# Optimization experiments

Measured on AMD Instinct MI355X. Metric: run time of the kernel, lower is better.

Reference implementation:

```python
import jax, jax.numpy as jnp
import numpy as np

N_NODES = 50000
N_EDGES = 600000
N_GRAPHS = 64
D_FEAT = 128
DIM_H = 128
N_HOPS = 3
OUT_DIM = 10


def setup_inputs() -> dict:
    key = jax.random.key(0)
    ks = jax.random.split(key, 16)
    x = jax.random.normal(ks[0], (N_NODES, D_FEAT), dtype=jnp.float32)
    edge_index = jax.random.randint(ks[1], (2, N_EDGES), 0, N_NODES, dtype=jnp.int64)
    batch = jnp.sort(jax.random.randint(ks[2], (N_NODES,), 0, N_GRAPHS, dtype=jnp.int64))
    def glorot(k, shape):
        fan = shape[0] + shape[1]
        return jax.random.uniform(k, shape, jnp.float32, -1.0, 1.0) * np.sqrt(6.0 / fan)
    # GCNConv weights stored as [in, out]; Linear weights stored as [in, out]
    W1 = glorot(ks[3], (D_FEAT, DIM_H)); b1 = jnp.zeros((DIM_H,), jnp.float32)
    W2 = glorot(ks[4], (DIM_H, DIM_H)); b2 = jnp.zeros((DIM_H,), jnp.float32)
    W3 = glorot(ks[5], (DIM_H, DIM_H)); b3 = jnp.zeros((DIM_H,), jnp.float32)
    H3 = DIM_H * N_HOPS
    lin1_W = glorot(ks[6], (H3, H3)); lin1_b = jnp.zeros((H3,), jnp.float32)
    lin2_W = glorot(ks[7], (H3, OUT_DIM)); lin2_b = jnp.zeros((OUT_DIM,), jnp.float32)
    return {"x": x, "W1": W1, "b1": b1, "W2": W2, "b2": b2, "W3": W3, "b3": b3,
            "lin1_W": lin1_W, "lin1_b": lin1_b, "lin2_W": lin2_W, "lin2_b": lin2_b,
            "edge_index": edge_index, "batch": batch}


def gcn_conv(x, W, b, src, dst, n_nodes):
    # PyG GCNConv (add_self_loops=True, normalize=True):
    #   deg[i] = in-degree at target + 1 (self loop); norm = d^-1/2[src] * d^-1/2[dst]
    deg = jnp.zeros((n_nodes,), x.dtype).at[dst].add(1.0) + 1.0
    dinv = jax.lax.rsqrt(deg)
    xw = x @ W  # [N, H] transform before propagate
    coef = (dinv[src] * dinv[dst])[:, None]
    agg = jnp.zeros_like(xw).at[dst].add(xw[src] * coef)
    agg = agg + xw * (dinv * dinv)[:, None]  # self-loop messages
    return agg + b


def global_mean_pool(h, batch, n_graphs):
    sums = jax.ops.segment_sum(h, batch, num_segments=n_graphs)
    cnt = jax.ops.segment_sum(jnp.ones((h.shape[0],), h.dtype), batch, num_segments=n_graphs)
    return sums / jnp.maximum(cnt, 1.0)[:, None]


def reference(x, W1, b1, W2, b2, W3, b3, lin1_W, lin1_b, lin2_W, lin2_b, edge_index, batch):
    src, dst = edge_index[0], edge_index[1]
    n = x.shape[0]
    h1 = gcn_conv(x, W1, b1, src, dst, n)
    h2 = gcn_conv(h1, W2, b2, src, dst, n)
    h3 = gcn_conv(h2, W3, b3, src, dst, n)
    pooled = jnp.concatenate([global_mean_pool(h, batch, N_GRAPHS) for h in (h1, h2, h3)], axis=1)
    h = jax.nn.relu(pooled @ lin1_W + lin1_b)
    # dropout is identity in eval mode
    h = h @ lin2_W + lin2_b
    return (h, jax.nn.log_softmax(h, axis=1))
```

## Files before the change

### kernel.cpp

```cpp
#include <hip/hip_runtime.h>
#include <hip/hip_fp16.h>
#include <math.h>

#define N_NODES 50000
#define N_EDGES 600000
#define N_GRAPHS 64
#define DFEAT 128
#define H3 384
#define OUTD 10
#define SCAN_BLOCKS 196
#define POOL_CHUNKS 16
#define APAD 136

typedef _Float16 f16x8 __attribute__((ext_vector_type(8)));
typedef float f32x4 __attribute__((ext_vector_type(4)));
typedef float f32x2 __attribute__((ext_vector_type(2)));

__global__ __launch_bounds__(256) void k_deg(const int* __restrict__ ei, int* __restrict__ deg,
                                             int* __restrict__ rank) {
    int e = blockIdx.x * 256 + threadIdx.x;
    if (e >= N_EDGES) return;
    int dst = ei[N_EDGES + e];
    rank[e] = atomicAdd(&deg[dst], 1);
}

__global__ __launch_bounds__(256) void k_part(const int* __restrict__ deg, int* __restrict__ part) {
    __shared__ int red[256];
    int tid = threadIdx.x;
    int i = blockIdx.x * 256 + tid;
    red[tid] = (i < N_NODES) ? deg[i] : 0;
    __syncthreads();
    for (int s = 128; s > 0; s >>= 1) {
        if (tid < s) red[tid] += red[tid + s];
        __syncthreads();
    }
    if (tid == 0) part[blockIdx.x] = red[0];
}

__global__ __launch_bounds__(256) void k_scanpart(const int* __restrict__ part, int* __restrict__ base) {
    __shared__ int buf[256];
    int tid = threadIdx.x;
    int v = (tid < SCAN_BLOCKS) ? part[tid] : 0;
    buf[tid] = v;
    __syncthreads();
    for (int d = 1; d < 256; d <<= 1) {
        int t = (tid >= d) ? buf[tid - d] : 0;
        __syncthreads();
        buf[tid] += t;
        __syncthreads();
    }
    if (tid < SCAN_BLOCKS) base[tid] = buf[tid] - v;
}

__global__ __launch_bounds__(256) void k_offsets(const int* __restrict__ deg, const int* __restrict__ base,
                                                 int* __restrict__ offs, float* __restrict__ dinv) {
    __shared__ int buf[256];
    int tid = threadIdx.x;
    int i = blockIdx.x * 256 + tid;
    int v = (i < N_NODES) ? deg[i] : 0;
    buf[tid] = v;
    __syncthreads();
    for (int d = 1; d < 256; d <<= 1) {
        int t = (tid >= d) ? buf[tid - d] : 0;
        __syncthreads();
        buf[tid] += t;
        __syncthreads();
    }
    if (i < N_NODES) {
        int excl = base[blockIdx.x] + buf[tid] - v;
        offs[i] = excl;
        dinv[i] = rsqrtf((float)v + 1.0f);
        if (i == N_NODES - 1) offs[N_NODES] = base[blockIdx.x] + buf[tid];
    }
}

__global__ __launch_bounds__(256) void k_fill(const int* __restrict__ ei, const int* __restrict__ offs,
                                              const int* __restrict__ rank, int* __restrict__ srcs) {
    int e = blockIdx.x * 256 + threadIdx.x;
    if (e >= N_EDGES) return;
    int s = ei[e];
    int t = ei[N_EDGES + e];
    srcs[offs[t] + rank[e]] = s;
}

__global__ __launch_bounds__(256) void k_prep(const float* __restrict__ W1, const float* __restrict__ W2,
                                              const float* __restrict__ W3, _Float16* __restrict__ Wt,
                                              float* __restrict__ pooled) {
    int b = blockIdx.x;
    if (b < 192) {
        int idx = b * 256 + threadIdx.x;
        int l = idx >> 14, r = idx & 16383;
        const float* W = (l == 0) ? W1 : (l == 1) ? W2 : W3;
        int k = r >> 7, n = r & 127;
        Wt[l * 16384 + n * 128 + k] = (_Float16)W[k * 128 + n];
    } else {
        int idx = (b - 192) * 256 + threadIdx.x;
        if (idx < N_GRAPHS * H3) pooled[idx] = 0.0f;
    }
}

template <bool A_FP16>
__global__ __launch_bounds__(256) void gemm_mfma(const void* __restrict__ Aptr, const _Float16* __restrict__ Wt,
                                                 unsigned char* __restrict__ T, int M) {
    __shared__ _Float16 As[64 * APAD];
    __shared__ _Float16 Ws[128 * APAD];
    int tid = threadIdx.x;
    int base = blockIdx.x * 64;
    for (int c = tid; c < 2048; c += 256) {
        int n = c >> 4, c8 = (c & 15) << 3;
        *(f16x8*)&Ws[n * APAD + c8] = *(const f16x8*)&Wt[n * 128 + c8];
    }
    for (int c = tid; c < 1024; c += 256) {
        int r = c >> 4, c8 = (c & 15) << 3;
        int gr = base + r; if (gr >= M) gr = M - 1;
        if (A_FP16) {
            const _Float16* A = (const _Float16*)Aptr;
            *(f16x8*)&As[r * APAD + c8] = *(const f16x8*)&A[(size_t)gr * 128 + c8];
        } else {
            const float* A = (const float*)Aptr;
            const float* src = A + (size_t)gr * 128 + c8;
            float4 v0 = *(const float4*)(src);
            float4 v1 = *(const float4*)(src + 4);
            f16x8 h;
            h[0] = (_Float16)v0.x; h[1] = (_Float16)v0.y; h[2] = (_Float16)v0.z; h[3] = (_Float16)v0.w;
            h[4] = (_Float16)v1.x; h[5] = (_Float16)v1.y; h[6] = (_Float16)v1.z; h[7] = (_Float16)v1.w;
            *(f16x8*)&As[r * APAD + c8] = h;
        }
    }
    __syncthreads();
    int wave = tid >> 6, lane = tid & 63;
    int m = lane & 15, quad = lane >> 4;
    f32x4 acc[8];
#pragma unroll
    for (int ct = 0; ct < 8; ++ct) acc[ct] = (f32x4){0.f, 0.f, 0.f, 0.f};
#pragma unroll
    for (int kc = 0; kc < 4; ++kc) {
        f16x8 a = *(const f16x8*)&As[(wave * 16 + m) * APAD + kc * 32 + quad * 8];
#pragma unroll
        for (int ct = 0; ct < 8; ++ct) {
            f16x8 b = *(const f16x8*)&Ws[(ct * 16 + m) * APAD + kc * 32 + quad * 8];
            acc[ct] = __builtin_amdgcn_mfma_f32_16x16x32_f16(b, a, acc[ct], 0, 0, 0);
        }
    }
    int node = base + wave * 16 + m;
    if (node < M) {
#pragma unroll
        for (int ct = 0; ct < 8; ++ct) {
            int col = ct * 16 + quad * 4;
            int p = __builtin_amdgcn_cvt_pk_fp8_f32(acc[ct][0], acc[ct][1], 0, false);
            p     = __builtin_amdgcn_cvt_pk_fp8_f32(acc[ct][2], acc[ct][3], p, true);
            *(int*)(T + (size_t)node * 128 + col) = p;
        }
    }
}

__global__ __launch_bounds__(128) void gather_agg(const unsigned short* __restrict__ T8,
                                                  const int* __restrict__ srcs,
                                                  const int* __restrict__ offs,
                                                  const float* __restrict__ dinv, const float* __restrict__ bias,
                                                  __half2* __restrict__ H2) {
    int node = blockIdx.x * 2 + (threadIdx.x >> 6);
    int lane = threadIdx.x & 63;
    if (node >= N_NODES) return;
    float di = dinv[node];
    float2 b2 = *(const float2*)(bias + lane * 2);
    f32x2 sf = __builtin_amdgcn_cvt_pk_f32_fp8((int)T8[(size_t)node * 64 + lane], false);
    float sx = 0.0f, sy = 0.0f;
    int lo = offs[node], hi = offs[node + 1];
    int e = lo;
    for (; e + 8 <= hi; e += 8) {
        int s0 = srcs[e + 0], s1 = srcs[e + 1], s2 = srcs[e + 2], s3 = srcs[e + 3];
        int s4 = srcs[e + 4], s5 = srcs[e + 5], s6 = srcs[e + 6], s7 = srcs[e + 7];
        float c0 = dinv[s0], c1 = dinv[s1], c2 = dinv[s2], c3 = dinv[s3];
        float c4 = dinv[s4], c5 = dinv[s5], c6 = dinv[s6], c7 = dinv[s7];
        int u0 = T8[(size_t)s0 * 64 + lane];
        int u1 = T8[(size_t)s1 * 64 + lane];
        int u2 = T8[(size_t)s2 * 64 + lane];
        int u3 = T8[(size_t)s3 * 64 + lane];
        int u4 = T8[(size_t)s4 * 64 + lane];
        int u5 = T8[(size_t)s5 * 64 + lane];
        int u6 = T8[(size_t)s6 * 64 + lane];
        int u7 = T8[(size_t)s7 * 64 + lane];
        f32x2 t0 = __builtin_amdgcn_cvt_pk_f32_fp8(u0, false);
        f32x2 t1 = __builtin_amdgcn_cvt_pk_f32_fp8(u1, false);
        f32x2 t2 = __builtin_amdgcn_cvt_pk_f32_fp8(u2, false);
        f32x2 t3 = __builtin_amdgcn_cvt_pk_f32_fp8(u3, false);
        f32x2 t4 = __builtin_amdgcn_cvt_pk_f32_fp8(u4, false);
        f32x2 t5 = __builtin_amdgcn_cvt_pk_f32_fp8(u5, false);
        f32x2 t6 = __builtin_amdgcn_cvt_pk_f32_fp8(u6, false);
        f32x2 t7 = __builtin_amdgcn_cvt_pk_f32_fp8(u7, false);
        sx += t0.x * c0; sy += t0.y * c0;
        sx += t1.x * c1; sy += t1.y * c1;
        sx += t2.x * c2; sy += t2.y * c2;
        sx += t3.x * c3; sy += t3.y * c3;
        sx += t4.x * c4; sy += t4.y * c4;
        sx += t5.x * c5; sy += t5.y * c5;
        sx += t6.x * c6; sy += t6.y * c6;
        sx += t7.x * c7; sy += t7.y * c7;
    }
    for (; e + 4 <= hi; e += 4) {
        int s0 = srcs[e + 0], s1 = srcs[e + 1], s2 = srcs[e + 2], s3 = srcs[e + 3];
        float c0 = dinv[s0], c1 = dinv[s1], c2 = dinv[s2], c3 = dinv[s3];
        f32x2 t0 = __builtin_amdgcn_cvt_pk_f32_fp8((int)T8[(size_t)s0 * 64 + lane], false);
        f32x2 t1 = __builtin_amdgcn_cvt_pk_f32_fp8((int)T8[(size_t)s1 * 64 + lane], false);
        f32x2 t2 = __builtin_amdgcn_cvt_pk_f32_fp8((int)T8[(size_t)s2 * 64 + lane], false);
        f32x2 t3 = __builtin_amdgcn_cvt_pk_f32_fp8((int)T8[(size_t)s3 * 64 + lane], false);
        sx += t0.x * c0; sy += t0.y * c0;
        sx += t1.x * c1; sy += t1.y * c1;
        sx += t2.x * c2; sy += t2.y * c2;
        sx += t3.x * c3; sy += t3.y * c3;
    }
    for (; e < hi; ++e) {
        int s = srcs[e];
        float c = dinv[s];
        f32x2 t = __builtin_amdgcn_cvt_pk_f32_fp8((int)T8[(size_t)s * 64 + lane], false);
        sx += t.x * c; sy += t.y * c;
    }
    float accx = di * sx + sf.x * (di * di) + b2.x;
    float accy = di * sy + sf.y * (di * di) + b2.y;
    H2[(size_t)node * 64 + lane] = __floats2half2_rn(accx, accy);
}

__global__ __launch_bounds__(256) void pool_kernel(const __half2* __restrict__ H2, const int* __restrict__ batch,
                                                   float* __restrict__ pooled, int colOff) {
    __shared__ int bounds[2];
    __shared__ float2 red[256];
    int g = blockIdx.x >> 4;
    int chunk = blockIdx.x & (POOL_CHUNKS - 1);
    int tid = threadIdx.x;
    int d2 = tid & 63, sub = tid >> 6;
    if (tid < 2) {
        int target = g + tid;
        int lo = 0, hi = N_NODES;
        while (lo < hi) {
            int mid = (lo + hi) >> 1;
            if (batch[mid] < target) lo = mid + 1; else hi = mid;
        }
        bounds[tid] = lo;
    }
    __syncthreads();
    int lo = bounds[0], hi = bounds[1];
    int n = hi - lo;
    int per = (n + POOL_CHUNKS - 1) / POOL_CHUNKS;
    int s = lo + chunk * per;
    int e = s + per; if (e > hi) e = hi;
    float ax = 0.0f, ay = 0.0f;
    for (int r = s + sub; r < e; r += 4) {
        float2 v = __half22float2(H2[(size_t)r * 64 + d2]);
        ax += v.x; ay += v.y;
    }
    red[tid] = make_float2(ax, ay);
    __syncthreads();
    if (sub == 0 && s < e) {
        float2 v0 = red[d2], v1 = red[64 + d2], v2 = red[128 + d2], v3 = red[192 + d2];
        float vx = v0.x + v1.x + v2.x + v3.x;
        float vy = v0.y + v1.y + v2.y + v3.y;
        atomicAdd(&pooled[g * H3 + colOff + d2 * 2],     vx);
        atomicAdd(&pooled[g * H3 + colOff + d2 * 2 + 1], vy);
    }
}

__global__ __launch_bounds__(384) void mlp_kernel(const float* __restrict__ pooled,
                                                  const int* __restrict__ batch,
                                                  const float* __restrict__ l1W, const float* __restrict__ l1b,
                                                  const float* __restrict__ l2W, const float* __restrict__ l2b,
                                                  float* __restrict__ out) {
    __shared__ float p[H3];
    __shared__ float hid[H3];
    __shared__ float o10[OUTD];
    __shared__ int bnd[2];
    int g = blockIdx.x, tid = threadIdx.x;
    if (tid < 2) {
        int target = g + tid;
        int lo = 0, hi = N_NODES;
        while (lo < hi) {
            int mid = (lo + hi) >> 1;
            if (batch[mid] < target) lo = mid + 1; else hi = mid;
        }
        bnd[tid] = lo;
    }
    __syncthreads();
    float inv = 1.0f / fmaxf((float)(bnd[1] - bnd[0]), 1.0f);
    p[tid] = pooled[g * H3 + tid] * inv;
    __syncthreads();
    float acc = l1b[tid];
    for (int k = 0; k < H3; ++k) acc += p[k] * l1W[k * H3 + tid];
    hid[tid] = fmaxf(acc, 0.0f);
    __syncthreads();
    if (tid < OUTD) {
        float o = l2b[tid];
        for (int k = 0; k < H3; ++k) o += hid[k] * l2W[k * OUTD + tid];
        o10[tid] = o;
        out[g * OUTD + tid] = o;
    }
    __syncthreads();
    if (tid == 0) {
        float m = o10[0];
        for (int j = 1; j < OUTD; ++j) m = fmaxf(m, o10[j]);
        float s = 0.0f;
        for (int j = 0; j < OUTD; ++j) s += expf(o10[j] - m);
        float lse = m + logf(s);
        for (int j = 0; j < OUTD; ++j) out[N_GRAPHS * OUTD + g * OUTD + j] = o10[j] - lse;
    }
}

extern "C" void kernel_launch(void* const* d_in, const int* in_sizes, int n_in,
                              void* d_out, int out_size, void* d_ws, size_t ws_size,
                              hipStream_t stream) {
    const float* x      = (const float*)d_in[0];
    const float* W1     = (const float*)d_in[1];
    const float* b1     = (const float*)d_in[2];
    const float* W2     = (const float*)d_in[3];
    const float* b2     = (const float*)d_in[4];
    const float* W3     = (const float*)d_in[5];
    const float* b3     = (const float*)d_in[6];
    const float* lin1_W = (const float*)d_in[7];
    const float* lin1_b = (const float*)d_in[8];
    const float* lin2_W = (const float*)d_in[9];
    const float* lin2_b = (const float*)d_in[10];
    const int* edge_index = (const int*)d_in[11];
    const int* batch      = (const int*)d_in[12];

    char* ws = (char*)d_ws;
    auto alloc = [&](size_t bytes) -> void* {
        void* p = (void*)ws;
        ws += (bytes + 255) & ~(size_t)255;
        return p;
    };
    int*   deg    = (int*)  alloc((size_t)N_NODES * 4);
    int*   part   = (int*)  alloc((size_t)SCAN_BLOCKS * 4);
    int*   pbase  = (int*)  alloc((size_t)SCAN_BLOCKS * 4);
    int*   offs   = (int*)  alloc((size_t)(N_NODES + 1) * 4);
    int*   rank   = (int*)  alloc((size_t)N_EDGES * 4);
    float* dinv   = (float*)alloc((size_t)N_NODES * 4);
    int*   srcs   = (int*)  alloc((size_t)N_EDGES * 4);
    unsigned char* T = (unsigned char*)alloc((size_t)N_NODES * 128);
    __half* H     = (__half*)alloc((size_t)N_NODES * 128 * 2);
    _Float16* Wt  = (_Float16*)alloc((size_t)3 * 128 * 128 * 2);
    float* pooled = (float*)alloc((size_t)N_GRAPHS * H3 * 4);

    hipMemsetAsync(deg, 0, (size_t)N_NODES * 4, stream);
    k_deg<<<(N_EDGES + 255) / 256, 256, 0, stream>>>(edge_index, deg, rank);
    k_part<<<SCAN_BLOCKS, 256, 0, stream>>>(deg, part);
    k_scanpart<<<1, 256, 0, stream>>>(part, pbase);
    k_offsets<<<SCAN_BLOCKS, 256, 0, stream>>>(deg, pbase, offs, dinv);
    k_fill<<<(N_EDGES + 255) / 256, 256, 0, stream>>>(edge_index, offs, rank, srcs);
    k_prep<<<288, 256, 0, stream>>>(W1, W2, W3, Wt, pooled);

    const float* bs[3] = {b1, b2, b3};
    for (int l = 0; l < 3; ++l) {
        if (l == 0)
            gemm_mfma<false><<<(N_NODES + 63) / 64, 256, 0, stream>>>(x, Wt, T, N_NODES);
        else
            gemm_mfma<true><<<(N_NODES + 63) / 64, 256, 0, stream>>>(H, Wt + (size_t)l * 16384, T, N_NODES);
        gather_agg<<<(N_NODES + 1) / 2, 128, 0, stream>>>((const unsigned short*)T, srcs, offs, dinv, bs[l], (__half2*)H);
        pool_kernel<<<N_GRAPHS * POOL_CHUNKS, 256, 0, stream>>>((const __half2*)H, batch, pooled, l * 128);
    }
    mlp_kernel<<<N_GRAPHS, 384, 0, stream>>>(pooled, batch, lin1_W, lin1_b, lin2_W, lin2_b, (float*)d_out);
}
```

Baseline: 306.2 us.

## Fuse CSR graph preprocessing kernels into one cooperative kernel with grid syncs

```diff
diff --git a/kernel.cpp b/kernel.cpp
--- a/kernel.cpp
+++ b/kernel.cpp
@@ -1,6 +1,9 @@
 #include <hip/hip_runtime.h>
 #include <hip/hip_fp16.h>
+#include <hip/hip_cooperative_groups.h>
 #include <math.h>
+
+namespace cg = cooperative_groups;
 
 #define N_NODES 50000
 #define N_EDGES 600000
@@ -16,31 +19,46 @@
 typedef float f32x4 __attribute__((ext_vector_type(4)));
 typedef float f32x2 __attribute__((ext_vector_type(2)));
 
-__global__ __launch_bounds__(256) void k_deg(const int* __restrict__ ei, int* __restrict__ deg,
-                                             int* __restrict__ rank) {
-    int e = blockIdx.x * 256 + threadIdx.x;
-    if (e >= N_EDGES) return;
-    int dst = ei[N_EDGES + e];
-    rank[e] = atomicAdd(&deg[dst], 1);
-}
-
-__global__ __launch_bounds__(256) void k_part(const int* __restrict__ deg, int* __restrict__ part) {
+__global__ __launch_bounds__(256) void k_graphprep(const int* __restrict__ ei, int* __restrict__ deg,
+                                                   int* __restrict__ rank, int* __restrict__ part,
+                                                   int* __restrict__ offs, float* __restrict__ dinv,
+                                                   int* __restrict__ srcs) {
+    cg::grid_group grid = cg::this_grid();
     __shared__ int red[256];
-    int tid = threadIdx.x;
-    int i = blockIdx.x * 256 + tid;
+    __shared__ int buf[256];
+    int tid = threadIdx.x, bid = blockIdx.x;
+    int gthreads = gridDim.x * 256;
+    int gtid = bid * 256 + tid;
+    for (int i = gtid; i < N_NODES; i += gthreads) deg[i] = 0;
+    grid.sync();
+    for (int e = gtid; e < N_EDGES; e += gthreads) {
+        int dst = ei[N_EDGES + e];
+        rank[e] = atomicAdd(&deg[dst], 1);
+    }
+    grid.sync();
+    int i = bid * 256 + tid;
     red[tid] = (i < N_NODES) ? deg[i] : 0;
     __syncthreads();
     for (int s = 128; s > 0; s >>= 1) {
         if (tid < s) red[tid] += red[tid + s];
         __syncthreads();
     }
-    if (tid == 0) part[blockIdx.x] = red[0];
-}
-
-__global__ __launch_bounds__(256) void k_scanpart(const int* __restrict__ part, int* __restrict__ base) {
-    __shared__ int buf[256];
-    int tid = threadIdx.x;
-    int v = (tid < SCAN_BLOCKS) ? part[tid] : 0;
+    if (tid == 0) part[bid] = red[0];
+    grid.sync();
+    if (bid == 0) {
+        int v = (tid < SCAN_BLOCKS) ? part[tid] : 0;
+        buf[tid] = v;
+        __syncthreads();
+        for (int d = 1; d < 256; d <<= 1) {
+            int t = (tid >= d) ? buf[tid - d] : 0;
+            __syncthreads();
+            buf[tid] += t;
+            __syncthreads();
+        }
+        if (tid < SCAN_BLOCKS) part[tid] = buf[tid] - v;
+    }
+    grid.sync();
+    int v = (i < N_NODES) ? deg[i] : 0;
     buf[tid] = v;
     __syncthreads();
     for (int d = 1; d < 256; d <<= 1) {
@@ -49,38 +67,18 @@
         buf[tid] += t;
         __syncthreads();
     }
-    if (tid < SCAN_BLOCKS) base[tid] = buf[tid] - v;
-}
-
-__global__ __launch_bounds__(256) void k_offsets(const int* __restrict__ deg, const int* __restrict__ base,
-                                                 int* __restrict__ offs, float* __restrict__ dinv) {
-    __shared__ int buf[256];
-    int tid = threadIdx.x;
-    int i = blockIdx.x * 256 + tid;
-    int v = (i < N_NODES) ? deg[i] : 0;
-    buf[tid] = v;
-    __syncthreads();
-    for (int d = 1; d < 256; d <<= 1) {
-        int t = (tid >= d) ? buf[tid - d] : 0;
-        __syncthreads();
-        buf[tid] += t;
-        __syncthreads();
-    }
     if (i < N_NODES) {
-        int excl = base[blockIdx.x] + buf[tid] - v;
+        int excl = part[bid] + buf[tid] - v;
         offs[i] = excl;
         dinv[i] = rsqrtf((float)v + 1.0f);
-        if (i == N_NODES - 1) offs[N_NODES] = base[blockIdx.x] + buf[tid];
-    }
-}
-
-__global__ __launch_bounds__(256) void k_fill(const int* __restrict__ ei, const int* __restrict__ offs,
-                                              const int* __restrict__ rank, int* __restrict__ srcs) {
-    int e = blockIdx.x * 256 + threadIdx.x;
-    if (e >= N_EDGES) return;
-    int s = ei[e];
-    int t = ei[N_EDGES + e];
-    srcs[offs[t] + rank[e]] = s;
+        if (i == N_NODES - 1) offs[N_NODES] = part[bid] + buf[tid];
+    }
+    grid.sync();
+    for (int e = gtid; e < N_EDGES; e += gthreads) {
+        int s = ei[e];
+        int t = ei[N_EDGES + e];
+        srcs[offs[t] + rank[e]] = s;
+    }
 }
 
 __global__ __launch_bounds__(256) void k_prep(const float* __restrict__ W1, const float* __restrict__ W2,
@@ -329,7 +327,6 @@
     };
     int*   deg    = (int*)  alloc((size_t)N_NODES * 4);
     int*   part   = (int*)  alloc((size_t)SCAN_BLOCKS * 4);
-    int*   pbase  = (int*)  alloc((size_t)SCAN_BLOCKS * 4);
     int*   offs   = (int*)  alloc((size_t)(N_NODES + 1) * 4);
     int*   rank   = (int*)  alloc((size_t)N_EDGES * 4);
     float* dinv   = (float*)alloc((size_t)N_NODES * 4);
@@ -339,12 +336,12 @@
     _Float16* Wt  = (_Float16*)alloc((size_t)3 * 128 * 128 * 2);
     float* pooled = (float*)alloc((size_t)N_GRAPHS * H3 * 4);
 
-    hipMemsetAsync(deg, 0, (size_t)N_NODES * 4, stream);
-    k_deg<<<(N_EDGES + 255) / 256, 256, 0, stream>>>(edge_index, deg, rank);
-    k_part<<<SCAN_BLOCKS, 256, 0, stream>>>(deg, part);
-    k_scanpart<<<1, 256, 0, stream>>>(part, pbase);
-    k_offsets<<<SCAN_BLOCKS, 256, 0, stream>>>(deg, pbase, offs, dinv);
-    k_fill<<<(N_EDGES + 255) / 256, 256, 0, stream>>>(edge_index, offs, rank, srcs);
+    {
+        void* args[] = {(void*)&edge_index, (void*)&deg, (void*)&rank, (void*)&part,
+                        (void*)&offs, (void*)&dinv, (void*)&srcs};
+        hipLaunchCooperativeKernel((const void*)k_graphprep, dim3(SCAN_BLOCKS), dim3(256),
+                                   args, 0, stream);
+    }
     k_prep<<<288, 256, 0, stream>>>(W1, W2, W3, Wt, pooled);
 
     const float* bs[3] = {b1, b2, b3};
```

New measurement: 436.2 us. 1.42x slower.

## Pack src index with fp16 coefficient and split waves across two edges per gather

Applied to the files above, without the earlier changes.

```diff
diff --git a/kernel.cpp b/kernel.cpp
--- a/kernel.cpp
+++ b/kernel.cpp
@@ -75,12 +75,14 @@
 }
 
 __global__ __launch_bounds__(256) void k_fill(const int* __restrict__ ei, const int* __restrict__ offs,
-                                              const int* __restrict__ rank, int* __restrict__ srcs) {
+                                              const int* __restrict__ rank, const float* __restrict__ dinv,
+                                              unsigned int* __restrict__ epack) {
     int e = blockIdx.x * 256 + threadIdx.x;
     if (e >= N_EDGES) return;
     int s = ei[e];
     int t = ei[N_EDGES + e];
-    srcs[offs[t] + rank[e]] = s;
+    unsigned short dh = __half_as_ushort(__float2half(dinv[s]));
+    epack[offs[t] + rank[e]] = (unsigned int)s | ((unsigned int)dh << 16);
 }
 
 __global__ __launch_bounds__(256) void k_prep(const float* __restrict__ W1, const float* __restrict__ W2,
@@ -154,71 +156,63 @@
     }
 }
 
-__global__ __launch_bounds__(128) void gather_agg(const unsigned short* __restrict__ T8,
-                                                  const int* __restrict__ srcs,
+__global__ __launch_bounds__(128) void gather_agg(const unsigned int* __restrict__ T32,
+                                                  const unsigned int* __restrict__ epack,
                                                   const int* __restrict__ offs,
                                                   const float* __restrict__ dinv, const float* __restrict__ bias,
                                                   __half2* __restrict__ H2) {
     int node = blockIdx.x * 2 + (threadIdx.x >> 6);
     int lane = threadIdx.x & 63;
+    int half = lane >> 5, l32 = lane & 31;
     if (node >= N_NODES) return;
     float di = dinv[node];
-    float2 b2 = *(const float2*)(bias + lane * 2);
-    f32x2 sf = __builtin_amdgcn_cvt_pk_f32_fp8((int)T8[(size_t)node * 64 + lane], false);
-    float sx = 0.0f, sy = 0.0f;
+    float a0 = 0.f, a1 = 0.f, a2 = 0.f, a3 = 0.f;
     int lo = offs[node], hi = offs[node + 1];
-    int e = lo;
-    for (; e + 8 <= hi; e += 8) {
-        int s0 = srcs[e + 0], s1 = srcs[e + 1], s2 = srcs[e + 2], s3 = srcs[e + 3];
-        int s4 = srcs[e + 4], s5 = srcs[e + 5], s6 = srcs[e + 6], s7 = srcs[e + 7];
-        float c0 = dinv[s0], c1 = dinv[s1], c2 = dinv[s2], c3 = dinv[s3];
-        float c4 = dinv[s4], c5 = dinv[s5], c6 = dinv[s6], c7 = dinv[s7];
-        int u0 = T8[(size_t)s0 * 64 + lane];
-        int u1 = T8[(size_t)s1 * 64 + lane];
-        int u2 = T8[(size_t)s2 * 64 + lane];
-        int u3 = T8[(size_t)s3 * 64 + lane];
-        int u4 = T8[(size_t)s4 * 64 + lane];
-        int u5 = T8[(size_t)s5 * 64 + lane];
-        int u6 = T8[(size_t)s6 * 64 + lane];
-        int u7 = T8[(size_t)s7 * 64 + lane];
-        f32x2 t0 = __builtin_amdgcn_cvt_pk_f32_fp8(u0, false);
-        f32x2 t1 = __builtin_amdgcn_cvt_pk_f32_fp8(u1, false);
-        f32x2 t2 = __builtin_amdgcn_cvt_pk_f32_fp8(u2, false);
-        f32x2 t3 = __builtin_amdgcn_cvt_pk_f32_fp8(u3, false);
-        f32x2 t4 = __builtin_amdgcn_cvt_pk_f32_fp8(u4, false);
-        f32x2 t5 = __builtin_amdgcn_cvt_pk_f32_fp8(u5, false);
-        f32x2 t6 = __builtin_amdgcn_cvt_pk_f32_fp8(u6, false);
-        f32x2 t7 = __builtin_amdgcn_cvt_pk_f32_fp8(u7, false);
-        sx += t0.x * c0; sy += t0.y * c0;
-        sx += t1.x * c1; sy += t1.y * c1;
-        sx += t2.x * c2; sy += t2.y * c2;
-        sx += t3.x * c3; sy += t3.y * c3;
-        sx += t4.x * c4; sy += t4.y * c4;
-        sx += t5.x * c5; sy += t5.y * c5;
-        sx += t6.x * c6; sy += t6.y * c6;
-        sx += t7.x * c7; sy += t7.y * c7;
-    }
-    for (; e + 4 <= hi; e += 4) {
-        int s0 = srcs[e + 0], s1 = srcs[e + 1], s2 = srcs[e + 2], s3 = srcs[e + 3];
-        float c0 = dinv[s0], c1 = dinv[s1], c2 = dinv[s2], c3 = dinv[s3];
-        f32x2 t0 = __builtin_amdgcn_cvt_pk_f32_fp8((int)T8[(size_t)s0 * 64 + lane], false);
-        f32x2 t1 = __builtin_amdgcn_cvt_pk_f32_fp8((int)T8[(size_t)s1 * 64 + lane], false);
-        f32x2 t2 = __builtin_amdgcn_cvt_pk_f32_fp8((int)T8[(size_t)s2 * 64 + lane], false);
-        f32x2 t3 = __builtin_amdgcn_cvt_pk_f32_fp8((int)T8[(size_t)s3 * 64 + lane], false);
-        sx += t0.x * c0; sy += t0.y * c0;
-        sx += t1.x * c1; sy += t1.y * c1;
-        sx += t2.x * c2; sy += t2.y * c2;
-        sx += t3.x * c3; sy += t3.y * c3;
-    }
-    for (; e < hi; ++e) {
-        int s = srcs[e];
-        float c = dinv[s];
-        f32x2 t = __builtin_amdgcn_cvt_pk_f32_fp8((int)T8[(size_t)s * 64 + lane], false);
-        sx += t.x * c; sy += t.y * c;
-    }
-    float accx = di * sx + sf.x * (di * di) + b2.x;
-    float accy = di * sy + sf.y * (di * di) + b2.y;
-    H2[(size_t)node * 64 + lane] = __floats2half2_rn(accx, accy);
+    int e = lo + half;
+    for (; e + 7 <= hi; e += 8) {
+        unsigned p0 = epack[e + 0], p1 = epack[e + 2], p2 = epack[e + 4], p3 = epack[e + 6];
+        int s0 = p0 & 0xffff, s1 = p1 & 0xffff, s2 = p2 & 0xffff, s3 = p3 & 0xffff;
+        float c0 = __half2float(__ushort_as_half((unsigned short)(p0 >> 16)));
+        float c1 = __half2float(__ushort_as_half((unsigned short)(p1 >> 16)));
+        float c2 = __half2float(__ushort_as_half((unsigned short)(p2 >> 16)));
+        float c3 = __half2float(__ushort_as_half((unsigned short)(p3 >> 16)));
+        unsigned u0 = T32[(size_t)s0 * 32 + l32];
+        unsigned u1 = T32[(size_t)s1 * 32 + l32];
+        unsigned u2 = T32[(size_t)s2 * 32 + l32];
+        unsigned u3 = T32[(size_t)s3 * 32 + l32];
+        f32x2 lo0 = __builtin_amdgcn_cvt_pk_f32_fp8(u0, false), hi0 = __builtin_amdgcn_cvt_pk_f32_fp8(u0, true);
+        f32x2 lo1 = __builtin_amdgcn_cvt_pk_f32_fp8(u1, false), hi1 = __builtin_amdgcn_cvt_pk_f32_fp8(u1, true);
+        f32x2 lo2 = __builtin_amdgcn_cvt_pk_f32_fp8(u2, false), hi2 = __builtin_amdgcn_cvt_pk_f32_fp8(u2, true);
+        f32x2 lo3 = __builtin_amdgcn_cvt_pk_f32_fp8(u3, false), hi3 = __builtin_amdgcn_cvt_pk_f32_fp8(u3, true);
+        a0 += lo0.x * c0; a1 += lo0.y * c0; a2 += hi0.x * c0; a3 += hi0.y * c0;
+        a0 += lo1.x * c1; a1 += lo1.y * c1; a2 += hi1.x * c1; a3 += hi1.y * c1;
+        a0 += lo2.x * c2; a1 += lo2.y * c2; a2 += hi2.x * c2; a3 += hi2.y * c2;
+        a0 += lo3.x * c3; a1 += lo3.y * c3; a2 += hi3.x * c3; a3 += hi3.y * c3;
+    }
+    for (; e < hi; e += 2) {
+        unsigned p = epack[e];
+        int s = p & 0xffff;
+        float c = __half2float(__ushort_as_half((unsigned short)(p >> 16)));
+        unsigned u = T32[(size_t)s * 32 + l32];
+        f32x2 tl = __builtin_amdgcn_cvt_pk_f32_fp8(u, false), th = __builtin_amdgcn_cvt_pk_f32_fp8(u, true);
+        a0 += tl.x * c; a1 += tl.y * c; a2 += th.x * c; a3 += th.y * c;
+    }
+    a0 += __shfl_xor(a0, 32, 64);
+    a1 += __shfl_xor(a1, 32, 64);
+    a2 += __shfl_xor(a2, 32, 64);
+    a3 += __shfl_xor(a3, 32, 64);
+    if (half == 0) {
+        unsigned su = T32[(size_t)node * 32 + l32];
+        f32x2 sl = __builtin_amdgcn_cvt_pk_f32_fp8(su, false), sh = __builtin_amdgcn_cvt_pk_f32_fp8(su, true);
+        float4 b4 = *(const float4*)(bias + l32 * 4);
+        float dd = di * di;
+        float r0 = di * a0 + sl.x * dd + b4.x;
+        float r1 = di * a1 + sl.y * dd + b4.y;
+        float r2 = di * a2 + sh.x * dd + b4.z;
+        float r3 = di * a3 + sh.y * dd + b4.w;
+        H2[(size_t)node * 64 + l32 * 2]     = __floats2half2_rn(r0, r1);
+        H2[(size_t)node * 64 + l32 * 2 + 1] = __floats2half2_rn(r2, r3);
+    }
 }
 
 __global__ __launch_bounds__(256) void pool_kernel(const __half2* __restrict__ H2, const int* __restrict__ batch,
@@ -333,7 +327,7 @@
     int*   offs   = (int*)  alloc((size_t)(N_NODES + 1) * 4);
     int*   rank   = (int*)  alloc((size_t)N_EDGES * 4);
     float* dinv   = (float*)alloc((size_t)N_NODES * 4);
-    int*   srcs   = (int*)  alloc((size_t)N_EDGES * 4);
+    unsigned int* epack = (unsigned int*)alloc((size_t)N_EDGES * 4);
     unsigned char* T = (unsigned char*)alloc((size_t)N_NODES * 128);
     __half* H     = (__half*)alloc((size_t)N_NODES * 128 * 2);
     _Float16* Wt  = (_Float16*)alloc((size_t)3 * 128 * 128 * 2);
@@ -344,7 +338,7 @@
     k_part<<<SCAN_BLOCKS, 256, 0, stream>>>(deg, part);
     k_scanpart<<<1, 256, 0, stream>>>(part, pbase);
     k_offsets<<<SCAN_BLOCKS, 256, 0, stream>>>(deg, pbase, offs, dinv);
-    k_fill<<<(N_EDGES + 255) / 256, 256, 0, stream>>>(edge_index, offs, rank, srcs);
+    k_fill<<<(N_EDGES + 255) / 256, 256, 0, stream>>>(edge_index, offs, rank, dinv, epack);
     k_prep<<<288, 256, 0, stream>>>(W1, W2, W3, Wt, pooled);
 
     const float* bs[3] = {b1, b2, b3};
@@ -353,7 +347,7 @@
             gemm_mfma<false><<<(N_NODES + 63) / 64, 256, 0, stream>>>(x, Wt, T, N_NODES);
         else
             gemm_mfma<true><<<(N_NODES + 63) / 64, 256, 0, stream>>>(H, Wt + (size_t)l * 16384, T, N_NODES);
-        gather_agg<<<(N_NODES + 1) / 2, 128, 0, stream>>>((const unsigned short*)T, srcs, offs, dinv, bs[l], (__half2*)H);
+        gather_agg<<<(N_NODES + 1) / 2, 128, 0, stream>>>((const unsigned int*)T, epack, offs, dinv, bs[l], (__half2*)H);
         pool_kernel<<<N_GRAPHS * POOL_CHUNKS, 256, 0, stream>>>((const __half2*)H, batch, pooled, l * 128);
     }
     mlp_kernel<<<N_GRAPHS, 384, 0, stream>>>(pooled, batch, lin1_W, lin1_b, lin2_W, lin2_b, (float*)d_out);
```

After: 309.0 us. Within noise of the previous version (+0.9%).
